# Kernel optimization log

Measured on AMD Instinct MI355X. Metric: run time of the kernel, lower is better.

The kernel has to match this reference:

```python
import jax, jax.numpy as jnp
import numpy as np

N = 50000   # num_node
E = 1600000 # edge_size (N * avg_degree 32)
B = 64      # batch, hardcoded via repeat(64,1,1) in the torch module


def setup_inputs() -> dict:
    key = jax.random.key(0)
    k = jax.random.split(key, 8)
    return {
        "t": jax.random.normal(k[0], (1,), dtype=jnp.float32),
        "input": jax.random.normal(k[1], (B, N), dtype=jnp.float32),
        "edge_i": jax.random.randint(k[2], (E,), 0, N, dtype=jnp.int32),
        "edge_j": jax.random.randint(k[3], (E,), 0, N, dtype=jnp.int32),
        "weight_react": jax.random.normal(k[4], (1, E), dtype=jnp.float32) / 10.0,
        "weight_diff": jax.random.normal(k[5], (1, E), dtype=jnp.float32) / 1000.0,
        "bias_reaction": jax.random.normal(k[6], (1, N), dtype=jnp.float32) / 10.0,
        "bias_diffusion": jax.random.normal(k[7], (1, N), dtype=jnp.float32) / 10.0,
    }


def _lap_matvec(x, w, src, dst, n):
    # W[src_e, dst_e] = w_e (duplicates coalesce by sum, as torch sparse_coo_tensor does)
    # L = diag(colsum(W)) - W ; returns x @ L^T applied batched: out[b, v] = (L x[b])[v]
    col = jax.ops.segment_sum(w, dst, num_segments=n)                 # [N] column sums
    msg = jax.ops.segment_sum(w[:, None] * x[:, dst].T, src,
                              num_segments=n)                          # [N, B]
    return col[None, :] * x - msg.T                                   # [B, N]


def reference(t, input, edge_i, edge_j, weight_react, weight_diff,
              bias_reaction, bias_diffusion):
    x = input                                                          # [B, N]
    n = x.shape[1]
    # reaction Laplacian uses edges (i -> j); diffusion uses transposed (j -> i)
    reaction = _lap_matvec(x, weight_react[0], edge_i, edge_j, n) + bias_reaction
    diffusion = _lap_matvec(x, weight_diff[0], edge_j, edge_i, n) + bias_diffusion
    # up and down both True: tanh(reaction) + diffusion + input
    return jnp.tanh(reaction) + diffusion + x
```

## Files before the change

kernel.cpp:

```cpp
#include <hip/hip_runtime.h>
#include <hip/hip_fp16.h>


#define BKT_SHIFT 7
#define BKT_NODES 128
#define HALF_NODES 64
#define RCAP 4608
#define CAP 80
#define CH 4096
#define NBP 512

__device__ __forceinline__ unsigned bf16_rne(float f) {
    unsigned u = __float_as_uint(f);
    unsigned rb = (u >> 16) & 1u;
    u += 0x7FFFu + rb;
    return u >> 16;
}
__device__ __forceinline__ float bf16_lo(int y) {
    return __uint_as_float(((unsigned)y) << 16);
}
__device__ __forceinline__ float bf16_hi(int y) {
    return __uint_as_float((unsigned)y & 0xFFFF0000u);
}

__global__ void transpose_kernel(const float* __restrict__ x, __half* __restrict__ xth,
                                 int* __restrict__ gcur, int ngcur, int N) {
    __shared__ float tile[64][65];
    int v0 = blockIdx.x * 64;
    int tx = threadIdx.x;
    int ty = threadIdx.y;
    int flat = blockIdx.x * 1024 + ty * 64 + tx;
    if (flat < ngcur) gcur[flat] = 0;
    if (v0 + tx < N) {
        for (int b = ty; b < 64; b += 16)
            tile[tx][b] = x[b * N + v0 + tx];
    }
    __syncthreads();
    for (int vl = ty; vl < 64; vl += 16) {
        int v = v0 + vl;
        if (v < N)
            xth[(size_t)v * 64 + tx] = __float2half(tile[vl][tx]);
    }
}

__global__ void __launch_bounds__(512) partition_kernel(
        const int* __restrict__ ei, const int* __restrict__ ej,
        const float* __restrict__ wr, const float* __restrict__ wd,
        int* __restrict__ gcur, int2* __restrict__ runs,
        int E, int NB) {
    __shared__ int cnt[2 * NBP];
    __shared__ int base_a[2 * NBP];
    __shared__ int gb[2 * NBP];
    __shared__ int2 buf[2 * CH];

    int tid = threadIdx.x;
    int e0 = blockIdx.x * CH;
    int ch_len = min(CH, E - e0);
    if (ch_len <= 0) return;

    int my_i[8], my_j[8];
    unsigned my_w[8];
    #pragma unroll
    for (int k = 0; k < 8; ++k) {
        int t = tid + k * 512;
        if (t < ch_len) {
            int e = e0 + t;
            my_i[k] = ei[e];
            my_j[k] = ej[e];
            my_w[k] = (bf16_rne(wr[e]) << 16) | bf16_rne(wd[e]);
        } else {
            my_i[k] = -1;
        }
    }

    for (int b = tid; b < 2 * NBP; b += 512) cnt[b] = 0;
    __syncthreads();
    #pragma unroll
    for (int k = 0; k < 8; ++k) {
        if (my_i[k] >= 0) {
            atomicAdd(&cnt[my_i[k] >> BKT_SHIFT], 1);
            atomicAdd(&cnt[NBP + (my_j[k] >> BKT_SHIFT)], 1);
        }
    }
    __syncthreads();
    if (tid < 64) {
        int carry = 0;
        #pragma unroll
        for (int c = 0; c < (2 * NBP) / 64; ++c) {
            int idx = c * 64 + tid;
            int val = cnt[idx];
            int scan = val;
            for (int off = 1; off < 64; off <<= 1) {
                int n = __shfl_up(scan, off, 64);
                if (tid >= off) scan += n;
            }
            int excl = scan - val + carry;
            base_a[idx] = excl;
            cnt[idx] = excl;
            carry += __shfl(scan, 63, 64);
        }
    }
    __syncthreads();
    #pragma unroll
    for (int k = 0; k < 8; ++k) {
        if (my_i[k] >= 0) {
            int i = my_i[k], j = my_j[k];
            unsigned wv = my_w[k];
            int b0 = i >> BKT_SHIFT;
            int p0 = atomicAdd(&cnt[b0], 1);
            buf[p0] = make_int2((int)(((unsigned)b0 << 23) | ((unsigned)(i & 127) << 16) | (unsigned)j),
                                (int)wv);
            int b1 = j >> BKT_SHIFT;
            int p1 = atomicAdd(&cnt[NBP + b1], 1);
            buf[p1] = make_int2((int)(((unsigned)b1 << 23) | ((unsigned)(j & 127) << 16) | (unsigned)i),
                                (int)((wv << 16) | (wv >> 16)));
        }
    }
    __syncthreads();
    for (int cb = tid; cb < 2 * NBP; cb += 512) {
        int n = cnt[cb] - base_a[cb];
        if (n > 0) {
            int side = cb >> 9;
            int bkt = cb & (NBP - 1);
            gb[cb] = atomicAdd(&gcur[side * NB + bkt], n);
        }
    }
    __syncthreads();
    int total = 2 * ch_len;
    for (int t = tid; t < total; t += 512) {
        int2 p = buf[t];
        int side = (t >= ch_len) ? 1 : 0;
        int bkt = ((unsigned)p.x >> 23) & 0x1FF;
        int cb = side * NBP + bkt;
        int rank = gb[cb] + (t - base_a[cb]);
        if (rank < RCAP)
            runs[((size_t)(side * NB + bkt)) * RCAP + rank] = p;
    }
}

#define ACC8S(S0,S1,S2,S3,S4,S5,S6,S7, P, D)                              \
    {                                                                     \
        float wv_ = bf16_hi(P);                                           \
        float2 f_;                                                        \
        f_ = __half22float2(*(const __half2*)&(D).x);                     \
        S0 = fmaf(wv_, f_.x, S0); S1 = fmaf(wv_, f_.y, S1);               \
        f_ = __half22float2(*(const __half2*)&(D).y);                     \
        S2 = fmaf(wv_, f_.x, S2); S3 = fmaf(wv_, f_.y, S3);               \
        f_ = __half22float2(*(const __half2*)&(D).z);                     \
        S4 = fmaf(wv_, f_.x, S4); S5 = fmaf(wv_, f_.y, S5);               \
        f_ = __half22float2(*(const __half2*)&(D).w);                     \
        S6 = fmaf(wv_, f_.x, S6); S7 = fmaf(wv_, f_.y, S7);               \
    }

#define COMB3(A) { A += __shfl_xor(A, 8); A += __shfl_xor(A, 16); A += __shfl_xor(A, 32); }

__global__ void __launch_bounds__(512, 8) sortgather_kernel(
        const int* __restrict__ gcur, const int2* __restrict__ runs,
        const __half* __restrict__ xth,
        __half* __restrict__ msg, float* __restrict__ colsum,
        int NB, int N) {
    __shared__ int cur[HALF_NODES];
    __shared__ float csum[HALF_NODES];
    __shared__ int dst[HALF_NODES * CAP];

    int blk = blockIdx.x;
    int sb = blk >> 1;
    int h  = blk & 1;
    int side = (sb >= NB) ? 1 : 0;
    int b = sb - side * NB;
    int v0 = (b << BKT_SHIFT) + h * HALF_NODES;
    int len = min(gcur[sb], RCAP);
    size_t roff = (size_t)sb * RCAP;
    int tid = threadIdx.x;

    int2 my[9];
    #pragma unroll
    for (int k = 0; k < 9; ++k) {
        int t = tid + k * 512;
        if (t < len) {
            long long raw = __builtin_nontemporal_load((const long long*)(runs + roff + t));
            my[k].x = (int)(unsigned)(raw & 0xFFFFFFFFll);
            my[k].y = (int)(unsigned)((unsigned long long)raw >> 32);
        } else my[k].x = -1;
    }

    if (tid < HALF_NODES) { cur[tid] = 0; csum[tid] = 0.f; }
    {
        int4* d4 = (int4*)dst;
        for (int idx = tid; idx < (HALF_NODES * CAP) / 4; idx += 512)
            d4[idx] = make_int4(0, 0, 0, 0);
    }
    __syncthreads();
    #pragma unroll
    for (int k = 0; k < 9; ++k) {
        if (my[k].x != -1) {
            int dl = ((unsigned)my[k].x >> 16) & 0x7F;
            if ((dl >> 6) == h) {
                int dll = dl & (HALF_NODES - 1);
                int pos = atomicAdd(&cur[dll], 1);
                if (pos < CAP)
                    dst[dll * CAP + pos] =
                        (int)(((unsigned)my[k].y & 0xFFFF0000u) | ((unsigned)my[k].x & 0xFFFFu));
                atomicAdd(&csum[dll], bf16_lo(my[k].y));
            }
        }
    }
    __syncthreads();

    const uint4* __restrict__ xq = (const uint4*)xth;
    int lane = tid & 63;
    int g  = lane >> 3;
    int bl = lane & 7;
    int wid = tid >> 6;
    for (int t = 0; t < HALF_NODES / 8; t += 2) {
        int dllA = wid * (HALF_NODES / 8) + t;
        int dllB = dllA + 1;
        int vA = v0 + dllA;
        int vB = v0 + dllB;
        const int* payA = dst + dllA * CAP + g;
        const int* payB = dst + dllB * CAP + g;
        int noctA = (min(cur[dllA], CAP) + 7) >> 3;
        int noctB = (min(cur[dllB], CAP) + 7) >> 3;
        int noct = max(noctA, noctB);
        float a0 = 0.f, a1 = 0.f, a2 = 0.f, a3 = 0.f;
        float a4 = 0.f, a5 = 0.f, a6 = 0.f, a7 = 0.f;
        float c0 = 0.f, c1 = 0.f, c2 = 0.f, c3 = 0.f;
        float c4 = 0.f, c5 = 0.f, c6 = 0.f, c7 = 0.f;
        int o = 0;
        for (; o + 2 <= noct; o += 2) {
            int pA0 = payA[8 * o];
            int pA1 = payA[8 * o + 8];
            int pB0 = payB[8 * o];
            int pB1 = payB[8 * o + 8];
            uint4 dA0 = xq[(((size_t)((unsigned)pA0 & 0xFFFFu)) << 3) + bl];
            uint4 dA1 = xq[(((size_t)((unsigned)pA1 & 0xFFFFu)) << 3) + bl];
            uint4 dB0 = xq[(((size_t)((unsigned)pB0 & 0xFFFFu)) << 3) + bl];
            uint4 dB1 = xq[(((size_t)((unsigned)pB1 & 0xFFFFu)) << 3) + bl];
            ACC8S(a0,a1,a2,a3,a4,a5,a6,a7, pA0, dA0)
            ACC8S(a0,a1,a2,a3,a4,a5,a6,a7, pA1, dA1)
            ACC8S(c0,c1,c2,c3,c4,c5,c6,c7, pB0, dB0)
            ACC8S(c0,c1,c2,c3,c4,c5,c6,c7, pB1, dB1)
        }
        if (o < noct) {
            int pA0 = payA[8 * o];
            int pB0 = payB[8 * o];
            uint4 dA0 = xq[(((size_t)((unsigned)pA0 & 0xFFFFu)) << 3) + bl];
            uint4 dB0 = xq[(((size_t)((unsigned)pB0 & 0xFFFFu)) << 3) + bl];
            ACC8S(a0,a1,a2,a3,a4,a5,a6,a7, pA0, dA0)
            ACC8S(c0,c1,c2,c3,c4,c5,c6,c7, pB0, dB0)
        }
        COMB3(a0) COMB3(a1) COMB3(a2) COMB3(a3)
        COMB3(a4) COMB3(a5) COMB3(a6) COMB3(a7)
        COMB3(c0) COMB3(c1) COMB3(c2) COMB3(c3)
        COMB3(c4) COMB3(c5) COMB3(c6) COMB3(c7)
        if (vA < N && lane < 8) {
            __half2 h0 = __floats2half2_rn(a0, a1);
            __half2 h1 = __floats2half2_rn(a2, a3);
            __half2 h2 = __floats2half2_rn(a4, a5);
            __half2 h3 = __floats2half2_rn(a6, a7);
            uint4 st = make_uint4(*(unsigned*)&h0, *(unsigned*)&h1,
                                  *(unsigned*)&h2, *(unsigned*)&h3);
            *(uint4*)(msg + ((size_t)side * N + vA) * 64 + 8 * lane) = st;
        }
        if (vB < N && lane < 8) {
            __half2 h0 = __floats2half2_rn(c0, c1);
            __half2 h1 = __floats2half2_rn(c2, c3);
            __half2 h2 = __floats2half2_rn(c4, c5);
            __half2 h3 = __floats2half2_rn(c6, c7);
            uint4 st = make_uint4(*(unsigned*)&h0, *(unsigned*)&h1,
                                  *(unsigned*)&h2, *(unsigned*)&h3);
            *(uint4*)(msg + ((size_t)side * N + vB) * 64 + 8 * lane) = st;
        }
        if (lane == 0) {
            if (vA < N) colsum[(size_t)side * N + vA] = csum[dllA];
            if (vB < N) colsum[(size_t)side * N + vB] = csum[dllB];
        }
    }
}

__global__ void final_kernel(const float* __restrict__ x,
                             const __half* __restrict__ msg,
                             const float* __restrict__ colsum,
                             const float* __restrict__ br, const float* __restrict__ bd,
                             float* __restrict__ out, int N) {
    __shared__ float tr[64][65];
    __shared__ float td[64][65];
    int v0 = blockIdx.x * 64;
    int tx = threadIdx.x;
    int ty = threadIdx.y;
    for (int vl = ty; vl < 64; vl += 16) {
        int v = v0 + vl;
        if (v < N) {
            tr[vl][tx] = __half2float(msg[(size_t)v * 64 + tx]);
            td[vl][tx] = __half2float(msg[((size_t)N + v) * 64 + tx]);
        }
    }
    __syncthreads();
    int v = v0 + tx;
    if (v < N) {
        float cold = colsum[v];
        float colr = colsum[(size_t)N + v];
        float brv = br[v], bdv = bd[v];
        for (int b = ty; b < 64; b += 16) {
            float xv = x[b * N + v];
            float r = colr * xv - tr[tx][b] + brv;
            float d = cold * xv - td[tx][b] + bdv;
            out[b * N + v] = tanhf(r) + d + xv;
        }
    }
}

extern "C" void kernel_launch(void* const* d_in, const int* in_sizes, int n_in,
                              void* d_out, int out_size, void* d_ws, size_t ws_size,
                              hipStream_t stream) {
    const float* x  = (const float*)d_in[1];
    const int*   ei = (const int*)d_in[2];
    const int*   ej = (const int*)d_in[3];
    const float* wr = (const float*)d_in[4];
    const float* wd = (const float*)d_in[5];
    const float* br = (const float*)d_in[6];
    const float* bd = (const float*)d_in[7];
    float* out = (float*)d_out;

    int E = in_sizes[2];
    int N = in_sizes[6];
    int NB = (N + BKT_NODES - 1) >> BKT_SHIFT;
    (void)out_size; (void)ws_size; (void)n_in;

    char* w = (char*)d_ws;
    __half* xth = (__half*)w;    w += (size_t)N * 64 * 2;
    __half* msg = (__half*)w;    w += (size_t)2 * N * 64 * 2;
    float* colsum = (float*)w;   w += (size_t)2 * N * 4;
    int* gcur   = (int*)w;       w += (size_t)2 * NB * 4;
    w = (char*)(((uintptr_t)w + 15) & ~(uintptr_t)15);
    int2* runs  = (int2*)w;

    dim3 tb(64, 16);
    int ntiles = (N + 63) / 64;
    transpose_kernel<<<ntiles, tb, 0, stream>>>(x, xth, gcur, 2 * NB, N);

    int nchunks = (E + CH - 1) / CH;
    partition_kernel<<<nchunks, 512, 0, stream>>>(ei, ej, wr, wd, gcur, runs, E, NB);

    sortgather_kernel<<<4 * NB, 512, 0, stream>>>(gcur, runs, xth, msg, colsum, NB, N);

    final_kernel<<<ntiles, tb, 0, stream>>>(x, msg, colsum, br, bd, out, N);
}
```

Before: 190.3 us.

## Fuse transpose into partition kernel and process full buckets per sortgather block

Moves the x transpose/half-conversion into the partition kernel, using its shared buffer as the tile after edge loads have been issued, and zeroes the bucket counters with a memset in place of the removed transpose kernel. Sortgather now handles a whole 128-node bucket per 1024-thread block, so each run is read once instead of twice with half the entries filtered out. The aim is to save a kernel launch and the duplicate run reads. In exchange it adds a memset call, extra barriers in partition, and larger blocks that may lower occupancy.

```diff
diff --git a/kernel.cpp b/kernel.cpp
--- a/kernel.cpp
+++ b/kernel.cpp
@@ -4,7 +4,6 @@
 
 #define BKT_SHIFT 7
 #define BKT_NODES 128
-#define HALF_NODES 64
 #define RCAP 4608
 #define CAP 80
 #define CH 4096
@@ -23,31 +22,12 @@
     return __uint_as_float((unsigned)y & 0xFFFF0000u);
 }
 
-__global__ void transpose_kernel(const float* __restrict__ x, __half* __restrict__ xth,
-                                 int* __restrict__ gcur, int ngcur, int N) {
-    __shared__ float tile[64][65];
-    int v0 = blockIdx.x * 64;
-    int tx = threadIdx.x;
-    int ty = threadIdx.y;
-    int flat = blockIdx.x * 1024 + ty * 64 + tx;
-    if (flat < ngcur) gcur[flat] = 0;
-    if (v0 + tx < N) {
-        for (int b = ty; b < 64; b += 16)
-            tile[tx][b] = x[b * N + v0 + tx];
-    }
-    __syncthreads();
-    for (int vl = ty; vl < 64; vl += 16) {
-        int v = v0 + vl;
-        if (v < N)
-            xth[(size_t)v * 64 + tx] = __float2half(tile[vl][tx]);
-    }
-}
-
 __global__ void __launch_bounds__(512) partition_kernel(
+        const float* __restrict__ x, __half* __restrict__ xth,
         const int* __restrict__ ei, const int* __restrict__ ej,
         const float* __restrict__ wr, const float* __restrict__ wd,
         int* __restrict__ gcur, int2* __restrict__ runs,
-        int E, int NB) {
+        int E, int NB, int N, int ntiles) {
     __shared__ int cnt[2 * NBP];
     __shared__ int base_a[2 * NBP];
     __shared__ int gb[2 * NBP];
@@ -56,7 +36,6 @@
     int tid = threadIdx.x;
     int e0 = blockIdx.x * CH;
     int ch_len = min(CH, E - e0);
-    if (ch_len <= 0) return;
 
     int my_i[8], my_j[8];
     unsigned my_w[8];
@@ -72,6 +51,33 @@
             my_i[k] = -1;
         }
     }
+
+    {
+        float (*tile)[65] = (float (*)[65])buf;
+        int tx = tid & 63;
+        int ty = tid >> 6;
+        for (int tt = blockIdx.x; 2 * tt < ntiles; tt += gridDim.x) {
+            #pragma unroll
+            for (int hf = 0; hf < 2; ++hf) {
+                int ti = 2 * tt + hf;
+                if (ti >= ntiles) break;
+                int v0 = ti * 64;
+                __syncthreads();
+                if (v0 + tx < N) {
+                    for (int bb = ty; bb < 64; bb += 8)
+                        tile[tx][bb] = x[bb * N + v0 + tx];
+                }
+                __syncthreads();
+                for (int vl = ty; vl < 64; vl += 8) {
+                    int v = v0 + vl;
+                    if (v < N)
+                        xth[(size_t)v * 64 + tx] = __float2half(tile[vl][tx]);
+                }
+            }
+        }
+        __syncthreads();
+    }
+    if (ch_len <= 0) return;
 
     for (int b = tid; b < 2 * NBP; b += 512) cnt[b] = 0;
     __syncthreads();
@@ -154,29 +160,27 @@
 
 #define COMB3(A) { A += __shfl_xor(A, 8); A += __shfl_xor(A, 16); A += __shfl_xor(A, 32); }
 
-__global__ void __launch_bounds__(512, 8) sortgather_kernel(
+__global__ void __launch_bounds__(1024, 8) sortgather_kernel(
         const int* __restrict__ gcur, const int2* __restrict__ runs,
         const __half* __restrict__ xth,
         __half* __restrict__ msg, float* __restrict__ colsum,
         int NB, int N) {
-    __shared__ int cur[HALF_NODES];
-    __shared__ float csum[HALF_NODES];
-    __shared__ int dst[HALF_NODES * CAP];
-
-    int blk = blockIdx.x;
-    int sb = blk >> 1;
-    int h  = blk & 1;
+    __shared__ int cur[BKT_NODES];
+    __shared__ float csum[BKT_NODES];
+    __shared__ int dst[BKT_NODES * CAP];
+
+    int sb = blockIdx.x;
     int side = (sb >= NB) ? 1 : 0;
     int b = sb - side * NB;
-    int v0 = (b << BKT_SHIFT) + h * HALF_NODES;
+    int v0 = b << BKT_SHIFT;
     int len = min(gcur[sb], RCAP);
     size_t roff = (size_t)sb * RCAP;
     int tid = threadIdx.x;
 
-    int2 my[9];
-    #pragma unroll
-    for (int k = 0; k < 9; ++k) {
-        int t = tid + k * 512;
+    int2 my[5];
+    #pragma unroll
+    for (int k = 0; k < 5; ++k) {
+        int t = tid + k * 1024;
         if (t < len) {
             long long raw = __builtin_nontemporal_load((const long long*)(runs + roff + t));
             my[k].x = (int)(unsigned)(raw & 0xFFFFFFFFll);
@@ -184,25 +188,22 @@
         } else my[k].x = -1;
     }
 
-    if (tid < HALF_NODES) { cur[tid] = 0; csum[tid] = 0.f; }
+    if (tid < BKT_NODES) { cur[tid] = 0; csum[tid] = 0.f; }
     {
         int4* d4 = (int4*)dst;
-        for (int idx = tid; idx < (HALF_NODES * CAP) / 4; idx += 512)
+        for (int idx = tid; idx < (BKT_NODES * CAP) / 4; idx += 1024)
             d4[idx] = make_int4(0, 0, 0, 0);
     }
     __syncthreads();
     #pragma unroll
-    for (int k = 0; k < 9; ++k) {
+    for (int k = 0; k < 5; ++k) {
         if (my[k].x != -1) {
             int dl = ((unsigned)my[k].x >> 16) & 0x7F;
-            if ((dl >> 6) == h) {
-                int dll = dl & (HALF_NODES - 1);
-                int pos = atomicAdd(&cur[dll], 1);
-                if (pos < CAP)
-                    dst[dll * CAP + pos] =
-                        (int)(((unsigned)my[k].y & 0xFFFF0000u) | ((unsigned)my[k].x & 0xFFFFu));
-                atomicAdd(&csum[dll], bf16_lo(my[k].y));
-            }
+            int pos = atomicAdd(&cur[dl], 1);
+            if (pos < CAP)
+                dst[dl * CAP + pos] =
+                    (int)(((unsigned)my[k].y & 0xFFFF0000u) | ((unsigned)my[k].x & 0xFFFFu));
+            atomicAdd(&csum[dl], bf16_lo(my[k].y));
         }
     }
     __syncthreads();
@@ -212,8 +213,8 @@
     int g  = lane >> 3;
     int bl = lane & 7;
     int wid = tid >> 6;
-    for (int t = 0; t < HALF_NODES / 8; t += 2) {
-        int dllA = wid * (HALF_NODES / 8) + t;
+    for (int t = 0; t < 8; t += 2) {
+        int dllA = wid * 8 + t;
         int dllB = dllA + 1;
         int vA = v0 + dllA;
         int vB = v0 + dllB;
@@ -335,14 +336,16 @@
     w = (char*)(((uintptr_t)w + 15) & ~(uintptr_t)15);
     int2* runs  = (int2*)w;
 
+    int ntiles = (N + 63) / 64;
+    int nchunks = (E + CH - 1) / CH;
+
+    hipMemsetAsync(gcur, 0, (size_t)2 * NB * sizeof(int), stream);
+
+    partition_kernel<<<nchunks, 512, 0, stream>>>(x, xth, ei, ej, wr, wd,
+                                                  gcur, runs, E, NB, N, ntiles);
+
+    sortgather_kernel<<<2 * NB, 1024, 0, stream>>>(gcur, runs, xth, msg, colsum, NB, N);
+
     dim3 tb(64, 16);
-    int ntiles = (N + 63) / 64;
-    transpose_kernel<<<ntiles, tb, 0, stream>>>(x, xth, gcur, 2 * NB, N);
-
-    int nchunks = (E + CH - 1) / CH;
-    partition_kernel<<<nchunks, 512, 0, stream>>>(ei, ej, wr, wd, gcur, runs, E, NB);
-
-    sortgather_kernel<<<4 * NB, 512, 0, stream>>>(gcur, runs, xth, msg, colsum, NB, N);
-
     final_kernel<<<ntiles, tb, 0, stream>>>(x, msg, colsum, br, bd, out, N);
 }
```

New measurement: 197.8 us. 1.04x slower.

## Fuse gather and final epilogue into one kernel with shared-memory message tiles

Applied to the files above, without the earlier changes.

Merges the sort/gather kernel and the final elementwise kernel. Each block now processes both the reaction and diffusion sides for its 64 nodes and keeps the per-node messages and column sums in shared memory, no longer writing them to global memory. This removes the fp16 msg and colsum round trip and one kernel launch. In exchange the grid is halved, each block does both sides in sequence with extra syncs, and shared memory per block grows, which may lower occupancy and parallelism.

```diff
diff --git a/kernel.cpp b/kernel.cpp
--- a/kernel.cpp
+++ b/kernel.cpp
@@ -9,6 +9,7 @@
 #define CAP 80
 #define CH 4096
 #define NBP 512
+#define TP 66
 
 __device__ __forceinline__ unsigned bf16_rne(float f) {
     unsigned u = __float_as_uint(f);
@@ -154,158 +155,152 @@
 
 #define COMB3(A) { A += __shfl_xor(A, 8); A += __shfl_xor(A, 16); A += __shfl_xor(A, 32); }
 
-__global__ void __launch_bounds__(512, 8) sortgather_kernel(
+#define TILE8(TILE, DLL, S0,S1,S2,S3,S4,S5,S6,S7)                         \
+    {                                                                     \
+        __half2 h0 = __floats2half2_rn(S0, S1);                           \
+        __half2 h1 = __floats2half2_rn(S2, S3);                           \
+        __half2 h2 = __floats2half2_rn(S4, S5);                           \
+        __half2 h3 = __floats2half2_rn(S6, S7);                           \
+        unsigned* row_ = (unsigned*)&TILE[DLL][0];                        \
+        row_[4 * lane + 0] = *(unsigned*)&h0;                             \
+        row_[4 * lane + 1] = *(unsigned*)&h1;                             \
+        row_[4 * lane + 2] = *(unsigned*)&h2;                             \
+        row_[4 * lane + 3] = *(unsigned*)&h3;                             \
+    }
+
+__global__ void __launch_bounds__(512, 8) fused_kernel(
         const int* __restrict__ gcur, const int2* __restrict__ runs,
-        const __half* __restrict__ xth,
-        __half* __restrict__ msg, float* __restrict__ colsum,
-        int NB, int N) {
+        const __half* __restrict__ xth, const float* __restrict__ x,
+        const float* __restrict__ br, const float* __restrict__ bd,
+        float* __restrict__ out, int NB, int N) {
     __shared__ int cur[HALF_NODES];
-    __shared__ float csum[HALF_NODES];
+    __shared__ float cold_s[HALF_NODES];
+    __shared__ float colr_s[HALF_NODES];
     __shared__ int dst[HALF_NODES * CAP];
+    __shared__ unsigned short tmr[HALF_NODES][TP];
+    __shared__ unsigned short tmd[HALF_NODES][TP];
 
     int blk = blockIdx.x;
-    int sb = blk >> 1;
-    int h  = blk & 1;
-    int side = (sb >= NB) ? 1 : 0;
-    int b = sb - side * NB;
-    int v0 = (b << BKT_SHIFT) + h * HALF_NODES;
-    int len = min(gcur[sb], RCAP);
-    size_t roff = (size_t)sb * RCAP;
+    int bucket = blk >> 1;
+    int h = blk & 1;
+    int v0 = (bucket << BKT_SHIFT) + h * HALF_NODES;
     int tid = threadIdx.x;
-
-    int2 my[9];
-    #pragma unroll
-    for (int k = 0; k < 9; ++k) {
-        int t = tid + k * 512;
-        if (t < len) {
-            long long raw = __builtin_nontemporal_load((const long long*)(runs + roff + t));
-            my[k].x = (int)(unsigned)(raw & 0xFFFFFFFFll);
-            my[k].y = (int)(unsigned)((unsigned long long)raw >> 32);
-        } else my[k].x = -1;
-    }
-
-    if (tid < HALF_NODES) { cur[tid] = 0; csum[tid] = 0.f; }
-    {
-        int4* d4 = (int4*)dst;
-        for (int idx = tid; idx < (HALF_NODES * CAP) / 4; idx += 512)
-            d4[idx] = make_int4(0, 0, 0, 0);
-    }
-    __syncthreads();
-    #pragma unroll
-    for (int k = 0; k < 9; ++k) {
-        if (my[k].x != -1) {
-            int dl = ((unsigned)my[k].x >> 16) & 0x7F;
-            if ((dl >> 6) == h) {
-                int dll = dl & (HALF_NODES - 1);
-                int pos = atomicAdd(&cur[dll], 1);
-                if (pos < CAP)
-                    dst[dll * CAP + pos] =
-                        (int)(((unsigned)my[k].y & 0xFFFF0000u) | ((unsigned)my[k].x & 0xFFFFu));
-                atomicAdd(&csum[dll], bf16_lo(my[k].y));
-            }
-        }
-    }
-    __syncthreads();
-
-    const uint4* __restrict__ xq = (const uint4*)xth;
     int lane = tid & 63;
     int g  = lane >> 3;
     int bl = lane & 7;
     int wid = tid >> 6;
-    for (int t = 0; t < HALF_NODES / 8; t += 2) {
-        int dllA = wid * (HALF_NODES / 8) + t;
-        int dllB = dllA + 1;
-        int vA = v0 + dllA;
-        int vB = v0 + dllB;
-        const int* payA = dst + dllA * CAP + g;
-        const int* payB = dst + dllB * CAP + g;
-        int noctA = (min(cur[dllA], CAP) + 7) >> 3;
-        int noctB = (min(cur[dllB], CAP) + 7) >> 3;
-        int noct = max(noctA, noctB);
-        float a0 = 0.f, a1 = 0.f, a2 = 0.f, a3 = 0.f;
-        float a4 = 0.f, a5 = 0.f, a6 = 0.f, a7 = 0.f;
-        float c0 = 0.f, c1 = 0.f, c2 = 0.f, c3 = 0.f;
-        float c4 = 0.f, c5 = 0.f, c6 = 0.f, c7 = 0.f;
-        int o = 0;
-        for (; o + 2 <= noct; o += 2) {
-            int pA0 = payA[8 * o];
-            int pA1 = payA[8 * o + 8];
-            int pB0 = payB[8 * o];
-            int pB1 = payB[8 * o + 8];
-            uint4 dA0 = xq[(((size_t)((unsigned)pA0 & 0xFFFFu)) << 3) + bl];
-            uint4 dA1 = xq[(((size_t)((unsigned)pA1 & 0xFFFFu)) << 3) + bl];
-            uint4 dB0 = xq[(((size_t)((unsigned)pB0 & 0xFFFFu)) << 3) + bl];
-            uint4 dB1 = xq[(((size_t)((unsigned)pB1 & 0xFFFFu)) << 3) + bl];
-            ACC8S(a0,a1,a2,a3,a4,a5,a6,a7, pA0, dA0)
-            ACC8S(a0,a1,a2,a3,a4,a5,a6,a7, pA1, dA1)
-            ACC8S(c0,c1,c2,c3,c4,c5,c6,c7, pB0, dB0)
-            ACC8S(c0,c1,c2,c3,c4,c5,c6,c7, pB1, dB1)
-        }
-        if (o < noct) {
-            int pA0 = payA[8 * o];
-            int pB0 = payB[8 * o];
-            uint4 dA0 = xq[(((size_t)((unsigned)pA0 & 0xFFFFu)) << 3) + bl];
-            uint4 dB0 = xq[(((size_t)((unsigned)pB0 & 0xFFFFu)) << 3) + bl];
-            ACC8S(a0,a1,a2,a3,a4,a5,a6,a7, pA0, dA0)
-            ACC8S(c0,c1,c2,c3,c4,c5,c6,c7, pB0, dB0)
-        }
-        COMB3(a0) COMB3(a1) COMB3(a2) COMB3(a3)
-        COMB3(a4) COMB3(a5) COMB3(a6) COMB3(a7)
-        COMB3(c0) COMB3(c1) COMB3(c2) COMB3(c3)
-        COMB3(c4) COMB3(c5) COMB3(c6) COMB3(c7)
-        if (vA < N && lane < 8) {
-            __half2 h0 = __floats2half2_rn(a0, a1);
-            __half2 h1 = __floats2half2_rn(a2, a3);
-            __half2 h2 = __floats2half2_rn(a4, a5);
-            __half2 h3 = __floats2half2_rn(a6, a7);
-            uint4 st = make_uint4(*(unsigned*)&h0, *(unsigned*)&h1,
-                                  *(unsigned*)&h2, *(unsigned*)&h3);
-            *(uint4*)(msg + ((size_t)side * N + vA) * 64 + 8 * lane) = st;
-        }
-        if (vB < N && lane < 8) {
-            __half2 h0 = __floats2half2_rn(c0, c1);
-            __half2 h1 = __floats2half2_rn(c2, c3);
-            __half2 h2 = __floats2half2_rn(c4, c5);
-            __half2 h3 = __floats2half2_rn(c6, c7);
-            uint4 st = make_uint4(*(unsigned*)&h0, *(unsigned*)&h1,
-                                  *(unsigned*)&h2, *(unsigned*)&h3);
-            *(uint4*)(msg + ((size_t)side * N + vB) * 64 + 8 * lane) = st;
-        }
-        if (lane == 0) {
-            if (vA < N) colsum[(size_t)side * N + vA] = csum[dllA];
-            if (vB < N) colsum[(size_t)side * N + vB] = csum[dllB];
-        }
-    }
-}
-
-__global__ void final_kernel(const float* __restrict__ x,
-                             const __half* __restrict__ msg,
-                             const float* __restrict__ colsum,
-                             const float* __restrict__ br, const float* __restrict__ bd,
-                             float* __restrict__ out, int N) {
-    __shared__ float tr[64][65];
-    __shared__ float td[64][65];
-    int v0 = blockIdx.x * 64;
-    int tx = threadIdx.x;
-    int ty = threadIdx.y;
-    for (int vl = ty; vl < 64; vl += 16) {
-        int v = v0 + vl;
-        if (v < N) {
-            tr[vl][tx] = __half2float(msg[(size_t)v * 64 + tx]);
-            td[vl][tx] = __half2float(msg[((size_t)N + v) * 64 + tx]);
-        }
-    }
-    __syncthreads();
+    const uint4* __restrict__ xq = (const uint4*)xth;
+
+    if (tid < HALF_NODES) { cold_s[tid] = 0.f; colr_s[tid] = 0.f; }
+
+    #pragma unroll
+    for (int side = 0; side < 2; ++side) {
+        int sb = side * NB + bucket;
+        int len = min(gcur[sb], RCAP);
+        size_t roff = (size_t)sb * RCAP;
+
+        int2 my[9];
+        #pragma unroll
+        for (int k = 0; k < 9; ++k) {
+            int t = tid + k * 512;
+            if (t < len) {
+                long long raw = __builtin_nontemporal_load((const long long*)(runs + roff + t));
+                my[k].x = (int)(unsigned)(raw & 0xFFFFFFFFll);
+                my[k].y = (int)(unsigned)((unsigned long long)raw >> 32);
+            } else my[k].x = -1;
+        }
+
+        if (tid < HALF_NODES) cur[tid] = 0;
+        {
+            int4* d4 = (int4*)dst;
+            for (int idx = tid; idx < (HALF_NODES * CAP) / 4; idx += 512)
+                d4[idx] = make_int4(0, 0, 0, 0);
+        }
+        __syncthreads();
+        float* cs = side ? colr_s : cold_s;
+        #pragma unroll
+        for (int k = 0; k < 9; ++k) {
+            if (my[k].x != -1) {
+                int dl = ((unsigned)my[k].x >> 16) & 0x7F;
+                if ((dl >> 6) == h) {
+                    int dll = dl & (HALF_NODES - 1);
+                    int pos = atomicAdd(&cur[dll], 1);
+                    if (pos < CAP)
+                        dst[dll * CAP + pos] =
+                            (int)(((unsigned)my[k].y & 0xFFFF0000u) | ((unsigned)my[k].x & 0xFFFFu));
+                    atomicAdd(&cs[dll], bf16_lo(my[k].y));
+                }
+            }
+        }
+        __syncthreads();
+
+        for (int t = 0; t < HALF_NODES / 8; t += 2) {
+            int dllA = wid * (HALF_NODES / 8) + t;
+            int dllB = dllA + 1;
+            const int* payA = dst + dllA * CAP + g;
+            const int* payB = dst + dllB * CAP + g;
+            int noctA = (min(cur[dllA], CAP) + 7) >> 3;
+            int noctB = (min(cur[dllB], CAP) + 7) >> 3;
+            int noct = max(noctA, noctB);
+            float a0 = 0.f, a1 = 0.f, a2 = 0.f, a3 = 0.f;
+            float a4 = 0.f, a5 = 0.f, a6 = 0.f, a7 = 0.f;
+            float c0 = 0.f, c1 = 0.f, c2 = 0.f, c3 = 0.f;
+            float c4 = 0.f, c5 = 0.f, c6 = 0.f, c7 = 0.f;
+            int o = 0;
+            for (; o + 2 <= noct; o += 2) {
+                int pA0 = payA[8 * o];
+                int pA1 = payA[8 * o + 8];
+                int pB0 = payB[8 * o];
+                int pB1 = payB[8 * o + 8];
+                uint4 dA0 = xq[(((size_t)((unsigned)pA0 & 0xFFFFu)) << 3) + bl];
+                uint4 dA1 = xq[(((size_t)((unsigned)pA1 & 0xFFFFu)) << 3) + bl];
+                uint4 dB0 = xq[(((size_t)((unsigned)pB0 & 0xFFFFu)) << 3) + bl];
+                uint4 dB1 = xq[(((size_t)((unsigned)pB1 & 0xFFFFu)) << 3) + bl];
+                ACC8S(a0,a1,a2,a3,a4,a5,a6,a7, pA0, dA0)
+                ACC8S(a0,a1,a2,a3,a4,a5,a6,a7, pA1, dA1)
+                ACC8S(c0,c1,c2,c3,c4,c5,c6,c7, pB0, dB0)
+                ACC8S(c0,c1,c2,c3,c4,c5,c6,c7, pB1, dB1)
+            }
+            if (o < noct) {
+                int pA0 = payA[8 * o];
+                int pB0 = payB[8 * o];
+                uint4 dA0 = xq[(((size_t)((unsigned)pA0 & 0xFFFFu)) << 3) + bl];
+                uint4 dB0 = xq[(((size_t)((unsigned)pB0 & 0xFFFFu)) << 3) + bl];
+                ACC8S(a0,a1,a2,a3,a4,a5,a6,a7, pA0, dA0)
+                ACC8S(c0,c1,c2,c3,c4,c5,c6,c7, pB0, dB0)
+            }
+            COMB3(a0) COMB3(a1) COMB3(a2) COMB3(a3)
+            COMB3(a4) COMB3(a5) COMB3(a6) COMB3(a7)
+            COMB3(c0) COMB3(c1) COMB3(c2) COMB3(c3)
+            COMB3(c4) COMB3(c5) COMB3(c6) COMB3(c7)
+            if (lane < 8) {
+                if (side == 0) {
+                    TILE8(tmr, dllA, a0,a1,a2,a3,a4,a5,a6,a7)
+                    TILE8(tmr, dllB, c0,c1,c2,c3,c4,c5,c6,c7)
+                } else {
+                    TILE8(tmd, dllA, a0,a1,a2,a3,a4,a5,a6,a7)
+                    TILE8(tmd, dllB, c0,c1,c2,c3,c4,c5,c6,c7)
+                }
+            }
+        }
+        __syncthreads();
+    }
+
+    int tx = lane;
     int v = v0 + tx;
     if (v < N) {
-        float cold = colsum[v];
-        float colr = colsum[(size_t)N + v];
+        float colr = colr_s[tx];
+        float cold = cold_s[tx];
         float brv = br[v], bdv = bd[v];
-        for (int b = ty; b < 64; b += 16) {
-            float xv = x[b * N + v];
-            float r = colr * xv - tr[tx][b] + brv;
-            float d = cold * xv - td[tx][b] + bdv;
-            out[b * N + v] = tanhf(r) + d + xv;
+        const __half* rr = (const __half*)&tmr[tx][0];
+        const __half* rd = (const __half*)&tmd[tx][0];
+        for (int b = wid; b < 64; b += 8) {
+            float xv = x[(size_t)b * N + v];
+            float mr = __half2float(rr[b]);
+            float md = __half2float(rd[b]);
+            float r2 = colr * xv - mr + brv;
+            float d2 = cold * xv - md + bdv;
+            out[(size_t)b * N + v] = tanhf(r2) + d2 + xv;
         }
     }
 }
@@ -329,8 +324,6 @@
 
     char* w = (char*)d_ws;
     __half* xth = (__half*)w;    w += (size_t)N * 64 * 2;
-    __half* msg = (__half*)w;    w += (size_t)2 * N * 64 * 2;
-    float* colsum = (float*)w;   w += (size_t)2 * N * 4;
     int* gcur   = (int*)w;       w += (size_t)2 * NB * 4;
     w = (char*)(((uintptr_t)w + 15) & ~(uintptr_t)15);
     int2* runs  = (int2*)w;
@@ -342,7 +335,5 @@
     int nchunks = (E + CH - 1) / CH;
     partition_kernel<<<nchunks, 512, 0, stream>>>(ei, ej, wr, wd, gcur, runs, E, NB);
 
-    sortgather_kernel<<<4 * NB, 512, 0, stream>>>(gcur, runs, xth, msg, colsum, NB, N);
-
-    final_kernel<<<ntiles, tb, 0, stream>>>(x, msg, colsum, br, bd, out, N);
-}
+    fused_kernel<<<2 * NB, 512, 0, stream>>>(gcur, runs, xth, x, br, bd, out, NB, N);
+}
```

New measurement: 209.6 us. 10.1% more time.
